# Kernel tuning notes

Hardware: AMD Instinct MI355X
Metric: run time of the kernel (lower is better)

Reference implementation:

```python
import jax, jax.numpy as jnp
import numpy as np

B, H, S, D = 1, 16, 8192, 64
WINDOW = 1024  # window_size from init; also used as the query block size


def setup_inputs() -> dict:
    key = jax.random.key(0)
    kq, kk, kv = jax.random.split(key, 3)
    Q = jax.random.normal(kq, (B, H, S, D), dtype=jnp.float32)
    K = jax.random.normal(kk, (B, H, S, D), dtype=jnp.float32)
    V = jax.random.normal(kv, (B, H, S, D), dtype=jnp.float32)
    return {"Q": Q, "K": K, "V": V}


def _sliding_window_attn(Q, K, V, window):
    # Banded causal attention: query q attends kv with 0 <= q - kv <= window.
    # Tile queries into blocks of size W=window; each query block i only needs
    # kv positions [i*W - W, i*W + W), i.e. a 2W-wide local slice. This honors
    # the block-sparse structure instead of materializing an SxS score matrix.
    b, h, s, d = Q.shape
    W = window
    nb = s // W  # number of query blocks
    # Pad K,V by W zeros at the front so every block slice is in-bounds.
    Kp = jnp.pad(K, ((0, 0), (0, 0), (W, 0), (0, 0)))
    Vp = jnp.pad(V, ((0, 0), (0, 0), (W, 0), (0, 0)))
    # Local kv indices for each block: block i covers padded positions [i*W, i*W+2W).
    idx = jnp.arange(nb)[:, None] * W + jnp.arange(2 * W)[None, :]  # [nb, 2W]
    Kb = Kp[:, :, idx, :]  # [B,H,nb,2W,D]
    Vb = Vp[:, :, idx, :]  # [B,H,nb,2W,D]
    Qb = Q.reshape(b, h, nb, W, d)  # [B,H,nb,W,D]

    scale = np.float32(1.0 / np.sqrt(d))  # flex_attention default scaling
    scores = jnp.einsum('bhnqd,bhnkd->bhnqk', Qb, Kb) * scale  # [B,H,nb,W,2W]

    # Global positions: q_global = i*W + qi ; kv_global = i*W + kj - W.
    # Mask conds: q>=kv  <=> qi >= kj - W ;  q-kv<=W  <=> qi <= kj ; kv_global>=0.
    qi = jnp.arange(W)[:, None]          # [W,1]
    kj = jnp.arange(2 * W)[None, :]      # [1,2W]
    rel_mask = (qi <= kj) & (qi >= kj - W)                        # [W,2W]
    kv_global = jnp.arange(nb)[:, None, None] * W + kj[None] - W  # [nb,1,2W]
    mask = rel_mask[None] & (kv_global >= 0)                      # [nb,W,2W]

    neg = jnp.finfo(scores.dtype).min
    scores = jnp.where(mask[None, None], scores, neg)
    attn = jax.nn.softmax(scores, axis=-1)
    out = jnp.einsum('bhnqk,bhnkd->bhnqd', attn, Vb)
    return out.reshape(b, h, s, d)


def reference(Q, K, V):
    return _sliding_window_attn(Q, K, V, WINDOW)
```

## Files before the change

### kernel.cpp

```cpp
#include <hip/hip_runtime.h>
#include <stdint.h>

namespace {
constexpr int kH = 16;
constexpr int kS = 8192;
constexpr int kD = 64;
constexpr int kW = 1024;

typedef __attribute__((ext_vector_type(4)))  float float4_t;
typedef __attribute__((ext_vector_type(16))) float f32x16;
typedef __attribute__((ext_vector_type(8)))  short bf16x8;
typedef __attribute__((ext_vector_type(8)))  short short8_t;

__device__ __forceinline__ unsigned short f2bf(float f) {
    union { float fv; uint32_t u; } c; c.fv = f;
    return (unsigned short)((c.u + 0x7fffu + ((c.u >> 16) & 1u)) >> 16);
}

__device__ __forceinline__ float fexp2(float x) {
#if __has_builtin(__builtin_amdgcn_exp2f)
    return __builtin_amdgcn_exp2f(x);
#else
    return exp2f(x);
#endif
}

__device__ __forceinline__ void gload16(const void* g, char* l) {
    __builtin_amdgcn_global_load_lds(
        (const __attribute__((address_space(1))) void*)g,
        (__attribute__((address_space(3))) void*)l, 16, 0, 0);
}

#define P_TO_FRAGS(P, U0, U1)                                                            \
    {                                                                                    \
        unsigned int wrd[8];                                                             \
        _Pragma("unroll")                                                                \
        for (int j = 0; j < 8; ++j)                                                      \
            asm("v_cvt_pk_bf16_f32 %0, %1, %2" : "=v"(wrd[j]) : "v"(P[2*j]), "v"(P[2*j+1])); \
        asm("v_permlane32_swap_b32 %0, %1" : "+v"(wrd[0]), "+v"(wrd[2]));                \
        asm("v_permlane32_swap_b32 %0, %1" : "+v"(wrd[1]), "+v"(wrd[3]));                \
        asm("v_permlane32_swap_b32 %0, %1" : "+v"(wrd[4]), "+v"(wrd[6]));                \
        asm("v_permlane32_swap_b32 %0, %1" : "+v"(wrd[5]), "+v"(wrd[7]));                \
        U0.u[0] = wrd[0]; U0.u[1] = wrd[1]; U0.u[2] = wrd[2]; U0.u[3] = wrd[3];          \
        U1.u[0] = wrd[4]; U1.u[1] = wrd[5]; U1.u[2] = wrd[6]; U1.u[3] = wrd[7];          \
    }

__global__ __launch_bounds__(256)
void prep_kv(const float* __restrict__ K, const float* __restrict__ V,
             unsigned short* __restrict__ Kb, unsigned short* __restrict__ Vt) {
    __shared__ float tile[64][65];
    const int h  = blockIdx.y;
    const int s0 = blockIdx.x * 64;
    const int tid = threadIdx.x;
    const size_t hb = (size_t)h * kS * kD;

    {
        const size_t base = hb + (size_t)s0 * kD + (size_t)tid * 16;
        float4_t a = *(const float4_t*)(K + base);
        float4_t b = *(const float4_t*)(K + base + 4);
        float4_t c = *(const float4_t*)(K + base + 8);
        float4_t d = *(const float4_t*)(K + base + 12);
        short8_t o0, o1;
        #pragma unroll
        for (int j = 0; j < 4; ++j) {
            o0[j] = (short)f2bf(a[j]); o0[j + 4] = (short)f2bf(b[j]);
            o1[j] = (short)f2bf(c[j]); o1[j + 4] = (short)f2bf(d[j]);
        }
        *(short8_t*)(Kb + base)     = o0;
        *(short8_t*)(Kb + base + 8) = o1;
    }

    #pragma unroll
    for (int it = 0; it < 4; ++it) {
        const int n = tid + it * 256;
        const int s = n >> 4, d0 = (n & 15) * 4;
        float4_t v = *(const float4_t*)(V + hb + (size_t)(s0 + s) * kD + d0);
        tile[s][d0 + 0] = v[0]; tile[s][d0 + 1] = v[1];
        tile[s][d0 + 2] = v[2]; tile[s][d0 + 3] = v[3];
    }
    __syncthreads();
    #pragma unroll
    for (int it = 0; it < 2; ++it) {
        const int n = tid + it * 256;
        const int d = n >> 3, sc = (n & 7) * 8;
        short8_t o;
        #pragma unroll
        for (int j = 0; j < 8; ++j) o[j] = (short)f2bf(tile[sc + j][d]);
        *(short8_t*)(Vt + (size_t)h * kD * kS + (size_t)d * kS + s0 + sc) = o;
    }
}

__global__ __launch_bounds__(256, 4)
void swa_main(const float* __restrict__ Qg, const unsigned short* __restrict__ Kb,
              const unsigned short* __restrict__ Vt, float* __restrict__ Og) {
    __shared__ __align__(16) char lds[2][16384];

    const int lid  = blockIdx.x;
    const int swz  = (lid & 7) * 128 + (lid >> 3);
    const int h    = swz >> 6;
    const int qblk = swz & 63;

    const int tid  = threadIdx.x;
    const int wv   = tid >> 6;
    const int lane = tid & 63;
    const int lq   = lane & 31;
    const int hi   = lane >> 5;

    const int q0b = qblk * 128;
    const int qs  = q0b + wv * 32;
    const int q   = qs + lq;
    const size_t hb  = (size_t)h * kS * kD;
    const size_t hbv = (size_t)h * kD * kS;

    constexpr float qscale = 0.125f * 1.44269504f;
    bf16x8 qf[4];
    {
        const float* qp = Qg + hb + (size_t)q * kD + hi * 8;
        #pragma unroll
        for (int c = 0; c < 4; ++c) {
            float4_t a = *(const float4_t*)(qp + c * 16);
            float4_t b = *(const float4_t*)(qp + c * 16 + 4);
            bf16x8 f;
            #pragma unroll
            for (int j = 0; j < 4; ++j) {
                f[j]     = (short)f2bf(a[j] * qscale);
                f[j + 4] = (short)f2bf(b[j] * qscale);
            }
            qf[c] = f;
        }
    }

    f32x16 acc[2];
    #pragma unroll
    for (int r = 0; r < 16; ++r) { acc[0][r] = 0.f; acc[1][r] = 0.f; }
    float l4[4] = {0.f, 0.f, 0.f, 0.f};

    const int kstart = (q0b >= kW) ? q0b - kW : 0;
    const int nt     = (q0b + 128 - kstart) >> 6;

    int srcK[2], srcV[2];
    #pragma unroll
    for (int i = 0; i < 2; ++i) {
        const int n = tid + i * 256;
        const int c = n ^ ((n >> 3) & 7);
        srcK[i] = (c >> 3) * 64 + (c & 7) * 8;
        srcV[i] = (c >> 3) * kS + (c & 7) * 8;
    }
    const unsigned short* KbH = Kb + hb;
    const unsigned short* VtH = Vt + hbv;

    auto stage = [&](int buf, int kb) {
        const unsigned short* Kt = KbH + (size_t)kb * 64;
        const unsigned short* Vq = VtH + kb;
        #pragma unroll
        for (int i = 0; i < 2; ++i) {
            const int db = i * 4096 + wv * 1024;
            gload16(Kt + srcK[i], &lds[buf][db]);
            gload16(Vq + srcV[i], &lds[buf][8192 + db]);
        }
    };

    union U { unsigned int u[4]; bf16x8 v; };

    stage(0, kstart);
    for (int t = 0; t < nt; ++t) {
        const int kb  = kstart + t * 64;
        const int kbn = (t + 1 < nt) ? kb + 64 : kb;
        stage((t + 1) & 1, kbn);
        asm volatile("s_waitcnt vmcnt(4)" ::: "memory");
        __builtin_amdgcn_s_barrier();
        asm volatile("" ::: "memory");

        const char* Kl = lds[t & 1];
        const char* Vl = lds[t & 1] + 8192;
        const int ksw = (lq & 7) << 4;

        const bool fast = (kb >= qs - 992) && (kb + 32 <= qs - 32);

        if (fast) {
            bf16x8 kf0[4], kf1[4], vf0[4], vf1[4];
            #pragma unroll
            for (int c = 0; c < 4; ++c) {
                kf0[c] = *(const bf16x8*)(Kl + ((lq * 128        + c * 32 + hi * 16) ^ ksw));
                kf1[c] = *(const bf16x8*)(Kl + (((32 + lq) * 128 + c * 32 + hi * 16) ^ ksw));
            }
            #pragma unroll
            for (int dh = 0; dh < 2; ++dh)
                #pragma unroll
                for (int kc = 0; kc < 2; ++kc) {
                    vf0[dh * 2 + kc] = *(const bf16x8*)(
                        Vl + (((dh * 32 + lq) * 128 + kc * 32 + hi * 16) ^ ksw));
                    vf1[dh * 2 + kc] = *(const bf16x8*)(
                        Vl + (((dh * 32 + lq) * 128 + 64 + kc * 32 + hi * 16) ^ ksw));
                }

            f32x16 st0, st1;
            #pragma unroll
            for (int r = 0; r < 16; ++r) { st0[r] = 0.f; st1[r] = 0.f; }
            #pragma unroll
            for (int c = 0; c < 4; ++c) {
                st0 = __builtin_amdgcn_mfma_f32_32x32x16_bf16(kf0[c], qf[c], st0, 0, 0, 0);
                st1 = __builtin_amdgcn_mfma_f32_32x32x16_bf16(kf1[c], qf[c], st1, 0, 0, 0);
            }

            float p0[16], p1[16];
            #pragma unroll
            for (int r = 0; r < 16; ++r) { p0[r] = fexp2(st0[r]); p1[r] = fexp2(st1[r]); }
            #pragma unroll
            for (int r = 0; r < 16; ++r) l4[r & 3] += p0[r] + p1[r];

            U a00, a01, a10, a11;
            P_TO_FRAGS(p0, a00, a01);
            P_TO_FRAGS(p1, a10, a11);

            acc[0] = __builtin_amdgcn_mfma_f32_32x32x16_bf16(vf0[0], a00.v, acc[0], 0, 0, 0);
            acc[1] = __builtin_amdgcn_mfma_f32_32x32x16_bf16(vf0[2], a00.v, acc[1], 0, 0, 0);
            acc[0] = __builtin_amdgcn_mfma_f32_32x32x16_bf16(vf0[1], a01.v, acc[0], 0, 0, 0);
            acc[1] = __builtin_amdgcn_mfma_f32_32x32x16_bf16(vf0[3], a01.v, acc[1], 0, 0, 0);
            acc[0] = __builtin_amdgcn_mfma_f32_32x32x16_bf16(vf1[0], a10.v, acc[0], 0, 0, 0);
            acc[1] = __builtin_amdgcn_mfma_f32_32x32x16_bf16(vf1[2], a10.v, acc[1], 0, 0, 0);
            acc[0] = __builtin_amdgcn_mfma_f32_32x32x16_bf16(vf1[1], a11.v, acc[0], 0, 0, 0);
            acc[1] = __builtin_amdgcn_mfma_f32_32x32x16_bf16(vf1[3], a11.v, acc[1], 0, 0, 0);
        } else {
            #pragma unroll
            for (int half = 0; half < 2; ++half) {
                const int kh = kb + half * 32;
                if (kh <= qs && kh >= qs - kW) {
                    const int krow = half * 32 + lq;
                    bf16x8 kf[4];
                    #pragma unroll
                    for (int c = 0; c < 4; ++c)
                        kf[c] = *(const bf16x8*)(Kl + ((krow * 128 + c * 32 + hi * 16) ^ ksw));

                    f32x16 st;
                    #pragma unroll
                    for (int r = 0; r < 16; ++r) st[r] = 0.f;
                    __builtin_amdgcn_s_setprio(1);
                    #pragma unroll
                    for (int c = 0; c < 4; ++c)
                        st = __builtin_amdgcn_mfma_f32_32x32x16_bf16(kf[c], qf[c], st, 0, 0, 0);
                    __builtin_amdgcn_s_setprio(0);

                    bf16x8 vf[4];
                    #pragma unroll
                    for (int dh = 0; dh < 2; ++dh)
                        #pragma unroll
                        for (int kc = 0; kc < 2; ++kc)
                            vf[dh * 2 + kc] = *(const bf16x8*)(
                                Vl + (((dh * 32 + lq) * 128 + half * 64 + kc * 32 + hi * 16) ^ ksw));

                    float p[16];
                    #pragma unroll
                    for (int r = 0; r < 16; ++r) {
                        const int ki = kh + (r & 3) + 8 * (r >> 2) + 4 * hi;
                        const bool ok = (ki <= q) && (ki + kW >= q);
                        const float e = fexp2(st[r]);
                        p[r] = ok ? e : 0.f;
                    }
                    #pragma unroll
                    for (int r = 0; r < 16; ++r) l4[r & 3] += p[r];

                    U u0, u1;
                    P_TO_FRAGS(p, u0, u1);

                    __builtin_amdgcn_s_setprio(1);
                    acc[0] = __builtin_amdgcn_mfma_f32_32x32x16_bf16(vf[0], u0.v, acc[0], 0, 0, 0);
                    acc[1] = __builtin_amdgcn_mfma_f32_32x32x16_bf16(vf[2], u0.v, acc[1], 0, 0, 0);
                    acc[0] = __builtin_amdgcn_mfma_f32_32x32x16_bf16(vf[1], u1.v, acc[0], 0, 0, 0);
                    acc[1] = __builtin_amdgcn_mfma_f32_32x32x16_bf16(vf[3], u1.v, acc[1], 0, 0, 0);
                    __builtin_amdgcn_s_setprio(0);
                }
            }
        }

        asm volatile("" ::: "memory");
        __builtin_amdgcn_s_barrier();
        asm volatile("" ::: "memory");
    }

    float l = (l4[0] + l4[1]) + (l4[2] + l4[3]);
    l += __shfl_xor(l, 32);
    const float rl = 1.f / l;
    float* op = Og + hb + (size_t)q * kD;
    #pragma unroll
    for (int g = 0; g < 4; ++g) {
        float4_t o0, o1;
        #pragma unroll
        for (int j = 0; j < 4; ++j) {
            o0[j] = acc[0][g * 4 + j] * rl;
            o1[j] = acc[1][g * 4 + j] * rl;
        }
        *(float4_t*)(op + g * 8 + hi * 4)      = o0;
        *(float4_t*)(op + 32 + g * 8 + hi * 4) = o1;
    }
}
}

extern "C" void kernel_launch(void* const* d_in, const int* in_sizes, int n_in,
                              void* d_out, int out_size, void* d_ws, size_t ws_size,
                              hipStream_t stream) {
    (void)in_sizes; (void)n_in; (void)out_size; (void)ws_size;
    const float* Q = (const float*)d_in[0];
    const float* K = (const float*)d_in[1];
    const float* V = (const float*)d_in[2];
    float* O = (float*)d_out;
    unsigned short* Kb = (unsigned short*)d_ws;
    unsigned short* Vt = Kb + (size_t)kH * kS * kD;

    prep_kv<<<dim3(kS / 64, kH), dim3(256), 0, stream>>>(K, V, Kb, Vt);
    swa_main<<<dim3(1024), dim3(256), 0, stream>>>(Q, Kb, Vt, O);
}
```

Before: 70.67 us.

## Pre-tile K and V into fragment-ordered 64-row blocks for contiguous LDS staging

The prep kernel now writes K and V as bf16 tiles per 64-key block, laid out in the exact order the MFMA fragments are read. The main kernel can then stage each tile with linear 16-byte loads and read LDS with constant offsets, with no XOR swizzle or per-thread source index math. The goal is fewer address ALU instructions, fully contiguous global loads for V (previously strided rows of length kS), and conflict-free LDS reads. The prep kernel gains an extra transpose pass through shared memory for K.

```diff
diff --git a/kernel.cpp b/kernel.cpp
--- a/kernel.cpp
+++ b/kernel.cpp
@@ -49,27 +49,33 @@
 void prep_kv(const float* __restrict__ K, const float* __restrict__ V,
              unsigned short* __restrict__ Kb, unsigned short* __restrict__ Vt) {
     __shared__ float tile[64][65];
-    const int h  = blockIdx.y;
-    const int s0 = blockIdx.x * 64;
+    const int h   = blockIdx.y;
+    const int tix = blockIdx.x;
+    const int s0  = tix * 64;
     const int tid = threadIdx.x;
     const size_t hb = (size_t)h * kS * kD;
-
-    {
-        const size_t base = hb + (size_t)s0 * kD + (size_t)tid * 16;
-        float4_t a = *(const float4_t*)(K + base);
-        float4_t b = *(const float4_t*)(K + base + 4);
-        float4_t c = *(const float4_t*)(K + base + 8);
-        float4_t d = *(const float4_t*)(K + base + 12);
-        short8_t o0, o1;
-        #pragma unroll
-        for (int j = 0; j < 4; ++j) {
-            o0[j] = (short)f2bf(a[j]); o0[j + 4] = (short)f2bf(b[j]);
-            o1[j] = (short)f2bf(c[j]); o1[j + 4] = (short)f2bf(d[j]);
-        }
-        *(short8_t*)(Kb + base)     = o0;
-        *(short8_t*)(Kb + base + 8) = o1;
-    }
-
+    unsigned short* Ko = Kb + hb + (size_t)tix * 4096;
+    unsigned short* Vo = Vt + hb + (size_t)tix * 4096;
+
+    #pragma unroll
+    for (int it = 0; it < 4; ++it) {
+        const int n = tid + it * 256;
+        const int s = n >> 4, d0 = (n & 15) * 4;
+        float4_t v = *(const float4_t*)(K + hb + (size_t)(s0 + s) * kD + d0);
+        tile[s][d0 + 0] = v[0]; tile[s][d0 + 1] = v[1];
+        tile[s][d0 + 2] = v[2]; tile[s][d0 + 3] = v[3];
+    }
+    __syncthreads();
+    #pragma unroll
+    for (int i = 0; i < 2; ++i) {
+        const int n = tid + i * 256;
+        const int g = n >> 6, r = n & 63;
+        short8_t o;
+        #pragma unroll
+        for (int j = 0; j < 8; ++j) o[j] = (short)f2bf(tile[r][g * 8 + j]);
+        *(short8_t*)(Ko + n * 8) = o;
+    }
+    __syncthreads();
     #pragma unroll
     for (int it = 0; it < 4; ++it) {
         const int n = tid + it * 256;
@@ -80,13 +86,13 @@
     }
     __syncthreads();
     #pragma unroll
-    for (int it = 0; it < 2; ++it) {
-        const int n = tid + it * 256;
-        const int d = n >> 3, sc = (n & 7) * 8;
+    for (int i = 0; i < 2; ++i) {
+        const int n = tid + i * 256;
+        const int g = n >> 6, r = n & 63;
         short8_t o;
         #pragma unroll
-        for (int j = 0; j < 8; ++j) o[j] = (short)f2bf(tile[sc + j][d]);
-        *(short8_t*)(Vt + (size_t)h * kD * kS + (size_t)d * kS + s0 + sc) = o;
+        for (int j = 0; j < 8; ++j) o[j] = (short)f2bf(tile[g * 8 + j][r]);
+        *(short8_t*)(Vo + n * 8) = o;
     }
 }
 
@@ -110,7 +116,6 @@
     const int qs  = q0b + wv * 32;
     const int q   = qs + lq;
     const size_t hb  = (size_t)h * kS * kD;
-    const size_t hbv = (size_t)h * kD * kS;
 
     constexpr float qscale = 0.125f * 1.44269504f;
     bf16x8 qf[4];
@@ -138,25 +143,18 @@
     const int kstart = (q0b >= kW) ? q0b - kW : 0;
     const int nt     = (q0b + 128 - kstart) >> 6;
 
-    int srcK[2], srcV[2];
-    #pragma unroll
-    for (int i = 0; i < 2; ++i) {
-        const int n = tid + i * 256;
-        const int c = n ^ ((n >> 3) & 7);
-        srcK[i] = (c >> 3) * 64 + (c & 7) * 8;
-        srcV[i] = (c >> 3) * kS + (c & 7) * 8;
-    }
     const unsigned short* KbH = Kb + hb;
-    const unsigned short* VtH = Vt + hbv;
+    const unsigned short* VtH = Vt + hb;
 
     auto stage = [&](int buf, int kb) {
-        const unsigned short* Kt = KbH + (size_t)kb * 64;
-        const unsigned short* Vq = VtH + kb;
+        const unsigned short* Kt = KbH + (size_t)(kb >> 6) * 4096;
+        const unsigned short* Vq = VtH + (size_t)(kb >> 6) * 4096;
         #pragma unroll
         for (int i = 0; i < 2; ++i) {
             const int db = i * 4096 + wv * 1024;
-            gload16(Kt + srcK[i], &lds[buf][db]);
-            gload16(Vq + srcV[i], &lds[buf][8192 + db]);
+            const int so = tid * 8 + i * 2048;
+            gload16(Kt + so, &lds[buf][db]);
+            gload16(Vq + so, &lds[buf][8192 + db]);
         }
     };
 
@@ -171,9 +169,8 @@
         __builtin_amdgcn_s_barrier();
         asm volatile("" ::: "memory");
 
-        const char* Kl = lds[t & 1];
-        const char* Vl = lds[t & 1] + 8192;
-        const int ksw = (lq & 7) << 4;
+        const char* Kl = lds[t & 1] + lq * 16 + hi * 1024;
+        const char* Vl = Kl + 8192;
 
         const bool fast = (kb >= qs - 992) && (kb + 32 <= qs - 32);
 
@@ -181,17 +178,15 @@
             bf16x8 kf0[4], kf1[4], vf0[4], vf1[4];
             #pragma unroll
             for (int c = 0; c < 4; ++c) {
-                kf0[c] = *(const bf16x8*)(Kl + ((lq * 128        + c * 32 + hi * 16) ^ ksw));
-                kf1[c] = *(const bf16x8*)(Kl + (((32 + lq) * 128 + c * 32 + hi * 16) ^ ksw));
+                kf0[c] = *(const bf16x8*)(Kl + c * 2048);
+                kf1[c] = *(const bf16x8*)(Kl + 512 + c * 2048);
             }
             #pragma unroll
             for (int dh = 0; dh < 2; ++dh)
                 #pragma unroll
                 for (int kc = 0; kc < 2; ++kc) {
-                    vf0[dh * 2 + kc] = *(const bf16x8*)(
-                        Vl + (((dh * 32 + lq) * 128 + kc * 32 + hi * 16) ^ ksw));
-                    vf1[dh * 2 + kc] = *(const bf16x8*)(
-                        Vl + (((dh * 32 + lq) * 128 + 64 + kc * 32 + hi * 16) ^ ksw));
+                    vf0[dh * 2 + kc] = *(const bf16x8*)(Vl + kc * 2048 + dh * 512);
+                    vf1[dh * 2 + kc] = *(const bf16x8*)(Vl + 4096 + kc * 2048 + dh * 512);
                 }
 
             f32x16 st0, st1;
@@ -226,11 +221,10 @@
             for (int half = 0; half < 2; ++half) {
                 const int kh = kb + half * 32;
                 if (kh <= qs && kh >= qs - kW) {
-                    const int krow = half * 32 + lq;
                     bf16x8 kf[4];
                     #pragma unroll
                     for (int c = 0; c < 4; ++c)
-                        kf[c] = *(const bf16x8*)(Kl + ((krow * 128 + c * 32 + hi * 16) ^ ksw));
+                        kf[c] = *(const bf16x8*)(Kl + half * 512 + c * 2048);
 
                     f32x16 st;
                     #pragma unroll
@@ -247,7 +241,7 @@
                         #pragma unroll
                         for (int kc = 0; kc < 2; ++kc)
                             vf[dh * 2 + kc] = *(const bf16x8*)(
-                                Vl + (((dh * 32 + lq) * 128 + half * 64 + kc * 32 + hi * 16) ^ ksw));
+                                Vl + half * 4096 + kc * 2048 + dh * 512);
 
                     float p[16];
                     #pragma unroll
```

New measurement: 71.44 us. Within noise of the previous version (+1.1%).

## Fuse K bf16 conversion into attention kernel via register-staged loads

Applied to the files above, without the earlier changes.

Removes the K fp32-to-bf16 conversion from the prep kernel, so only V is still converted and transposed there. The attention kernel now loads fp32 K tiles into registers one iteration ahead, converts them with packed bf16 instructions and writes them to swizzled LDS after compute. This cuts the workspace write and re-read of K and shrinks the prep kernel. In exchange K is read as fp32 once per query block, which doubles K load bytes, and the main loop takes on extra registers and VALU work.

```diff
diff --git a/kernel.cpp b/kernel.cpp
--- a/kernel.cpp
+++ b/kernel.cpp
@@ -11,6 +11,7 @@
 typedef __attribute__((ext_vector_type(16))) float f32x16;
 typedef __attribute__((ext_vector_type(8)))  short bf16x8;
 typedef __attribute__((ext_vector_type(8)))  short short8_t;
+typedef __attribute__((ext_vector_type(4)))  unsigned int u32x4;
 
 __device__ __forceinline__ unsigned short f2bf(float f) {
     union { float fv; uint32_t u; } c; c.fv = f;
@@ -46,30 +47,12 @@
     }
 
 __global__ __launch_bounds__(256)
-void prep_kv(const float* __restrict__ K, const float* __restrict__ V,
-             unsigned short* __restrict__ Kb, unsigned short* __restrict__ Vt) {
+void prep_v(const float* __restrict__ V, unsigned short* __restrict__ Vt) {
     __shared__ float tile[64][65];
     const int h  = blockIdx.y;
     const int s0 = blockIdx.x * 64;
     const int tid = threadIdx.x;
     const size_t hb = (size_t)h * kS * kD;
-
-    {
-        const size_t base = hb + (size_t)s0 * kD + (size_t)tid * 16;
-        float4_t a = *(const float4_t*)(K + base);
-        float4_t b = *(const float4_t*)(K + base + 4);
-        float4_t c = *(const float4_t*)(K + base + 8);
-        float4_t d = *(const float4_t*)(K + base + 12);
-        short8_t o0, o1;
-        #pragma unroll
-        for (int j = 0; j < 4; ++j) {
-            o0[j] = (short)f2bf(a[j]); o0[j + 4] = (short)f2bf(b[j]);
-            o1[j] = (short)f2bf(c[j]); o1[j + 4] = (short)f2bf(d[j]);
-        }
-        *(short8_t*)(Kb + base)     = o0;
-        *(short8_t*)(Kb + base + 8) = o1;
-    }
-
     #pragma unroll
     for (int it = 0; it < 4; ++it) {
         const int n = tid + it * 256;
@@ -86,12 +69,12 @@
         short8_t o;
         #pragma unroll
         for (int j = 0; j < 8; ++j) o[j] = (short)f2bf(tile[sc + j][d]);
-        *(short8_t*)(Vt + (size_t)h * kD * kS + (size_t)d * kS + s0 + sc) = o;
+        *(short8_t*)(Vt + hb + (size_t)d * kS + s0 + sc) = o;
     }
 }
 
 __global__ __launch_bounds__(256, 4)
-void swa_main(const float* __restrict__ Qg, const unsigned short* __restrict__ Kb,
+void swa_main(const float* __restrict__ Qg, const float* __restrict__ Kg,
               const unsigned short* __restrict__ Vt, float* __restrict__ Og) {
     __shared__ __align__(16) char lds[2][16384];
 
@@ -109,8 +92,7 @@
     const int q0b = qblk * 128;
     const int qs  = q0b + wv * 32;
     const int q   = qs + lq;
-    const size_t hb  = (size_t)h * kS * kD;
-    const size_t hbv = (size_t)h * kD * kS;
+    const size_t hb = (size_t)h * kS * kD;
 
     constexpr float qscale = 0.125f * 1.44269504f;
     bf16x8 qf[4];
@@ -138,36 +120,68 @@
     const int kstart = (q0b >= kW) ? q0b - kW : 0;
     const int nt     = (q0b + 128 - kstart) >> 6;
 
-    int srcK[2], srcV[2];
+    int kdst[2];
+    const int r0 = tid >> 3, g0 = tid & 7;
+    const int r1 = (tid + 256) >> 3, g1 = tid & 7;
+    kdst[0] = (r0 * 128 + g0 * 16) ^ ((r0 & 7) << 4);
+    kdst[1] = (r1 * 128 + g1 * 16) ^ ((r1 & 7) << 4);
+    const float* KgH = Kg + hb;
+
+    int srcV[2];
     #pragma unroll
     for (int i = 0; i < 2; ++i) {
         const int n = tid + i * 256;
         const int c = n ^ ((n >> 3) & 7);
-        srcK[i] = (c >> 3) * 64 + (c & 7) * 8;
         srcV[i] = (c >> 3) * kS + (c & 7) * 8;
     }
-    const unsigned short* KbH = Kb + hb;
-    const unsigned short* VtH = Vt + hbv;
-
-    auto stage = [&](int buf, int kb) {
-        const unsigned short* Kt = KbH + (size_t)kb * 64;
+    const unsigned short* VtH = Vt + hb;
+
+    float4_t kreg[2][2];
+    auto loadK = [&](int kb) {
+        const float* p0 = KgH + (size_t)(kb + r0) * kD + g0 * 8;
+        const float* p1 = KgH + (size_t)(kb + r1) * kD + g1 * 8;
+        kreg[0][0] = *(const float4_t*)(p0);
+        kreg[0][1] = *(const float4_t*)(p0 + 4);
+        kreg[1][0] = *(const float4_t*)(p1);
+        kreg[1][1] = *(const float4_t*)(p1 + 4);
+    };
+    auto stageV = [&](int buf, int kb) {
         const unsigned short* Vq = VtH + kb;
         #pragma unroll
+        for (int i = 0; i < 2; ++i)
+            gload16(Vq + srcV[i], &lds[buf][8192 + i * 4096 + wv * 1024]);
+    };
+    auto cvtWriteK = [&](int buf) {
+        #pragma unroll
         for (int i = 0; i < 2; ++i) {
-            const int db = i * 4096 + wv * 1024;
-            gload16(Kt + srcK[i], &lds[buf][db]);
-            gload16(Vq + srcV[i], &lds[buf][8192 + db]);
+            u32x4 w;
+            #pragma unroll
+            for (int j = 0; j < 2; ++j) {
+                unsigned int lo, hi2;
+                asm("v_cvt_pk_bf16_f32 %0, %1, %2" : "=v"(lo)
+                    : "v"(kreg[i][j][0]), "v"(kreg[i][j][1]));
+                asm("v_cvt_pk_bf16_f32 %0, %1, %2" : "=v"(hi2)
+                    : "v"(kreg[i][j][2]), "v"(kreg[i][j][3]));
+                w[j * 2]     = lo;
+                w[j * 2 + 1] = hi2;
+            }
+            *(u32x4*)(&lds[buf][kdst[i]]) = w;
         }
     };
 
     union U { unsigned int u[4]; bf16x8 v; };
 
-    stage(0, kstart);
+    loadK(kstart);
+    stageV(0, kstart);
+    asm volatile("s_waitcnt vmcnt(2)" ::: "memory");
+    cvtWriteK(0);
+
     for (int t = 0; t < nt; ++t) {
         const int kb  = kstart + t * 64;
         const int kbn = (t + 1 < nt) ? kb + 64 : kb;
-        stage((t + 1) & 1, kbn);
-        asm volatile("s_waitcnt vmcnt(4)" ::: "memory");
+        loadK(kbn);
+        stageV((t + 1) & 1, kbn);
+        asm volatile("s_waitcnt vmcnt(6) lgkmcnt(0)" ::: "memory");
         __builtin_amdgcn_s_barrier();
         asm volatile("" ::: "memory");
 
@@ -273,6 +287,9 @@
             }
         }
 
+        asm volatile("s_waitcnt vmcnt(2)" ::: "memory");
+        cvtWriteK((t + 1) & 1);
+
         asm volatile("" ::: "memory");
         __builtin_amdgcn_s_barrier();
         asm volatile("" ::: "memory");
@@ -304,9 +321,8 @@
     const float* K = (const float*)d_in[1];
     const float* V = (const float*)d_in[2];
     float* O = (float*)d_out;
-    unsigned short* Kb = (unsigned short*)d_ws;
-    unsigned short* Vt = Kb + (size_t)kH * kS * kD;
-
-    prep_kv<<<dim3(kS / 64, kH), dim3(256), 0, stream>>>(K, V, Kb, Vt);
-    swa_main<<<dim3(1024), dim3(256), 0, stream>>>(Q, Kb, Vt, O);
-}
+    unsigned short* Vt = (unsigned short*)d_ws;
+
+    prep_v<<<dim3(kS / 64, kH), dim3(256), 0, stream>>>(V, Vt);
+    swa_main<<<dim3(1024), dim3(256), 0, stream>>>(Q, K, Vt, O);
+}
```

Result: slower. 192.2 us (+172.0%).
